# Kernel optimization log

Hardware: AMD Instinct MI355X
Metric: run time of the kernel (lower is better)

Reference implementation:

```python
import jax, jax.numpy as jnp
import numpy as np

B, L, D = 4, 2048, 1024
H, DK, DV = 16, 64, 64


def setup_inputs() -> dict:
    key = jax.random.key(0)
    ks = jax.random.split(key, 11)
    s = 1.0 / np.sqrt(D)
    so = 1.0 / np.sqrt(H * DV)
    return {
        "query": jax.random.normal(ks[0], (B, L, D), jnp.float32),
        "key": jax.random.normal(ks[1], (B, L, D), jnp.float32),
        "value": jax.random.normal(ks[2], (B, L, D), jnp.float32),
        "W_q": jax.random.uniform(ks[3], (D, H * DK), jnp.float32, -s, s),
        "b_q": jax.random.uniform(ks[4], (H * DK,), jnp.float32, -s, s),
        "W_k": jax.random.uniform(ks[5], (D, H * DK), jnp.float32, -s, s),
        "b_k": jax.random.uniform(ks[6], (H * DK,), jnp.float32, -s, s),
        "W_v": jax.random.uniform(ks[7], (D, H * DV), jnp.float32, -s, s),
        "b_v": jax.random.uniform(ks[8], (H * DV,), jnp.float32, -s, s),
        "W_o": jax.random.uniform(ks[9], (H * DV, D), jnp.float32, -so, so),
        "b_o": jax.random.uniform(ks[10], (D,), jnp.float32, -so, so),
    }


def reference(query, key, value, W_q, b_q, W_k, b_k, W_v, b_v, W_o, b_o):
    # QKV projections, then split heads: [B, L, H*d] -> [B, H, L, d]
    q = (query @ W_q + b_q).reshape(B, L, H, DK).transpose(0, 2, 1, 3)
    k = (key @ W_k + b_k).reshape(B, L, H, DK).transpose(0, 2, 1, 3)
    v = (value @ W_v + b_v).reshape(B, L, H, DV).transpose(0, 2, 1, 3)
    # scaled dot-product attention: softmax(q k^T / sqrt(dk)) v
    scores = jnp.einsum("bhqd,bhkd->bhqk", q, k) / jnp.sqrt(jnp.float32(DK))
    attn = jax.nn.softmax(scores, axis=-1)
    ctx = jnp.einsum("bhqk,bhkd->bhqd", attn, v)
    # combine heads: [B, H, L, dv] -> [B, L, H*dv], output projection
    out = ctx.transpose(0, 2, 1, 3).reshape(B, L, H * DV) @ W_o + b_o
    return out
```

## Files before the change

### kernel.cpp

```cpp
#include <hip/hip_runtime.h>

#define BATCH 4
#define LSEQ 2048
#define DMODEL 1024
#define NHEAD 16
#define DHEAD 64
#define MTOT (BATCH * LSEQ)

typedef _Float16 f16;
typedef _Float16 f16x8 __attribute__((ext_vector_type(8)));
typedef _Float16 f16x4 __attribute__((ext_vector_type(4)));
typedef _Float16 f16x2 __attribute__((ext_vector_type(2)));
typedef float f32x4 __attribute__((ext_vector_type(4)));
typedef float f32x16 __attribute__((ext_vector_type(16)));
typedef unsigned int u32;
typedef unsigned int u32x4 __attribute__((ext_vector_type(4)));

#define SCORE_SCALE 0.180336878f

typedef const __attribute__((address_space(1))) void gvoid;
typedef __attribute__((address_space(3))) void lvoid;
#define GLDS16(g, l) __builtin_amdgcn_global_load_lds((gvoid*)(g), (lvoid*)(l), 16, 0, 0)

#define WAITCNT(s) do { asm volatile("s_waitcnt " s ::: "memory"); \
                        __builtin_amdgcn_sched_barrier(0); } while (0)
#define BAR() __builtin_amdgcn_s_barrier()

__global__ __launch_bounds__(256)
void cvt3_f32_f16(const float* __restrict__ in0, const float* __restrict__ in1,
                  const float* __restrict__ in2, f16* __restrict__ out, int n8)
{
    const int y = blockIdx.y;
    const float* in = (y == 0) ? in0 : (y == 1) ? in1 : in2;
    f16* o = out + (size_t)y * (size_t)n8 * 8;
    int i = blockIdx.x * 256 + threadIdx.x;
    if (i >= n8) return;
    float4 a = ((const float4*)in)[2 * i];
    float4 b = ((const float4*)in)[2 * i + 1];
    f16x8 v;
    v[0] = (f16)a.x; v[1] = (f16)a.y; v[2] = (f16)a.z; v[3] = (f16)a.w;
    v[4] = (f16)b.x; v[5] = (f16)b.y; v[6] = (f16)b.z; v[7] = (f16)b.w;
    ((f16x8*)o)[i] = v;
}

__global__ __launch_bounds__(256)
void wconv4(const float* __restrict__ W0, const float* __restrict__ W1,
            const float* __restrict__ W2, const float* __restrict__ W3,
            f16* __restrict__ WtBase)
{
    __shared__ float T[64][68];
    const int z = blockIdx.z;
    const float* W = (z == 0) ? W0 : (z == 1) ? W1 : (z == 2) ? W2 : W3;
    f16* Wt = WtBase + (size_t)z * DMODEL * DMODEL;
    const int t = threadIdx.x;
    const int k0 = blockIdx.y * 64, n0 = blockIdx.x * 64;
    const int tr = t >> 4, tc = (t & 15) * 4;
#pragma unroll
    for (int p = 0; p < 64; p += 16) {
        float4 v = *(const float4*)&W[(size_t)(k0 + tr + p) * DMODEL + n0 + tc];
        *(float4*)&T[tr + p][tc] = v;
    }
    __syncthreads();
    const int n = t >> 2, kc = (t & 3) * 16;
    f16x8 o0, o1;
#pragma unroll
    for (int j = 0; j < 8; ++j) o0[j] = (f16)T[kc + j][n];
#pragma unroll
    for (int j = 0; j < 8; ++j) o1[j] = (f16)T[kc + 8 + j][n];
    *(f16x8*)&Wt[(size_t)(n0 + n) * DMODEL + k0 + kc] = o0;
    *(f16x8*)&Wt[(size_t)(n0 + n) * DMODEL + k0 + kc + 8] = o1;
}

__global__ __launch_bounds__(512, 2)
void gemm_qkv_8ph(const f16* __restrict__ A, const f16* __restrict__ Bt,
                  const float* __restrict__ b0, const float* __restrict__ b1,
                  const float* __restrict__ b2, f16* __restrict__ Cout)
{
    __shared__ f16 As[2][2][128][64];
    __shared__ f16 Bs[2][2][128][64];

    const int t = threadIdx.x;
    const int lane = t & 63;
    const int w = t >> 6, wr = w >> 2, wc = w & 3;
    const int quad = lane >> 4, m16 = lane & 15;
    const int m0 = blockIdx.x * 256, n0 = blockIdx.y * 256;
    const int which = n0 >> 10;

    const int sr = t >> 3;
    const int sc = ((t & 7) << 4) ^ ((sr & 7) << 4);
    const f16* Asrc = A + (size_t)which * MTOT * DMODEL
                        + (size_t)(m0 + sr) * DMODEL + (sc >> 1);
    const f16* Bsrc = Bt + (size_t)(n0 + sr) * DMODEL + (sc >> 1);

    auto stA = [&](int buf, int h, int kt) {
        const f16* s = Asrc + (size_t)(h * 128) * DMODEL + kt * 64;
        GLDS16(s,               &As[buf][h][0][0] + t * 8);
        GLDS16(s + 64 * DMODEL, &As[buf][h][64][0] + t * 8);
    };
    auto stB = [&](int buf, int h, int kt) {
        const f16* s = Bsrc + (size_t)(h * 128) * DMODEL + kt * 64;
        GLDS16(s,               &Bs[buf][h][0][0] + t * 8);
        GLDS16(s + 64 * DMODEL, &Bs[buf][h][64][0] + t * 8);
    };

    const int fsw = (m16 & 7) << 4;
    auto rdA = [&](int buf, int mf, int ks) -> f16x8 {
        return *(const f16x8*)((const char*)&As[buf][wr][0][0]
                               + (mf * 16 + m16) * 128
                               + ((ks * 64 + quad * 16) ^ fsw));
    };
    auto rdB = [&](int buf, int nf, int ks) -> f16x8 {
        return *(const f16x8*)((const char*)&Bs[buf][wc >> 1][0][0]
                               + ((wc & 1) * 64 + nf * 16 + m16) * 128
                               + ((ks * 64 + quad * 16) ^ fsw));
    };

    f32x4 acc[8][4] = {};
    f16x8 af[4][2], bf[4][2];

    auto ldA = [&](int buf, int mg) {
#pragma unroll
        for (int mi = 0; mi < 4; ++mi)
#pragma unroll
            for (int ks = 0; ks < 2; ++ks)
                af[mi][ks] = rdA(buf, mg * 4 + mi, ks);
    };
    auto ldB = [&](int buf) {
#pragma unroll
        for (int nf = 0; nf < 4; ++nf)
#pragma unroll
            for (int ks = 0; ks < 2; ++ks)
                bf[nf][ks] = rdB(buf, nf, ks);
    };
    auto mfma16 = [&](int mg, int np) {
        __builtin_amdgcn_s_setprio(1);
#pragma unroll
        for (int mi = 0; mi < 4; ++mi)
#pragma unroll
            for (int ni = 0; ni < 2; ++ni)
#pragma unroll
                for (int ks = 0; ks < 2; ++ks)
                    acc[mg * 4 + mi][np * 2 + ni] =
                        __builtin_amdgcn_mfma_f32_16x16x32_f16(
                            af[mi][ks], bf[np * 2 + ni][ks],
                            acc[mg * 4 + mi][np * 2 + ni], 0, 0, 0);
        __builtin_amdgcn_s_setprio(0);
    };

    stB(0, 0, 0); stB(0, 1, 0); stA(0, 0, 0); stA(0, 1, 0);
    stB(1, 0, 1); stB(1, 1, 1); stA(1, 0, 1);
    WAITCNT("vmcnt(6)");
    BAR();
    __builtin_amdgcn_sched_barrier(0);

    const int NHI = (DMODEL / 128) - 1;
    for (int i = 0; i < NHI; ++i) {
        const int T1 = 2 * i + 1, T2 = 2 * i + 2, T3 = 2 * i + 3;
        ldA(0, 0); ldB(0);
        stA(1, 1, T1);
        BAR(); WAITCNT("lgkmcnt(0)");
        mfma16(0, 0);
        BAR(); __builtin_amdgcn_sched_barrier(0);
        stB(0, 0, T2);
        BAR(); WAITCNT("lgkmcnt(0)");
        mfma16(0, 1);
        BAR(); __builtin_amdgcn_sched_barrier(0);
        ldA(0, 1);
        stB(0, 1, T2);
        BAR(); WAITCNT("lgkmcnt(0)");
        mfma16(1, 0);
        BAR(); __builtin_amdgcn_sched_barrier(0);
        stA(0, 0, T2);
        WAITCNT("vmcnt(6)");
        BAR(); WAITCNT("lgkmcnt(0)");
        mfma16(1, 1);
        BAR(); __builtin_amdgcn_sched_barrier(0);
        ldA(1, 0); ldB(1);
        stA(0, 1, T2);
        BAR(); WAITCNT("lgkmcnt(0)");
        mfma16(0, 0);
        BAR(); __builtin_amdgcn_sched_barrier(0);
        stB(1, 0, T3);
        BAR(); WAITCNT("lgkmcnt(0)");
        mfma16(0, 1);
        BAR(); __builtin_amdgcn_sched_barrier(0);
        ldA(1, 1);
        stB(1, 1, T3);
        BAR(); WAITCNT("lgkmcnt(0)");
        mfma16(1, 0);
        BAR(); __builtin_amdgcn_sched_barrier(0);
        stA(1, 0, T3);
        WAITCNT("vmcnt(6)");
        BAR(); WAITCNT("lgkmcnt(0)");
        mfma16(1, 1);
        BAR(); __builtin_amdgcn_sched_barrier(0);
    }

    stA(1, 1, 2 * NHI + 1);
    WAITCNT("vmcnt(0)");
    BAR();
    ldA(0, 0); ldB(0); WAITCNT("lgkmcnt(0)");
    mfma16(0, 0); mfma16(0, 1);
    ldA(0, 1); WAITCNT("lgkmcnt(0)");
    mfma16(1, 0); mfma16(1, 1);
    ldA(1, 0); ldB(1); WAITCNT("lgkmcnt(0)");
    mfma16(0, 0); mfma16(0, 1);
    ldA(1, 1); WAITCNT("lgkmcnt(0)");
    mfma16(1, 0); mfma16(1, 1);

    const float* bp = (which == 0) ? b0 : (which == 1) ? b1 : b2;
    const float scale = (which == 0) ? SCORE_SCALE : 1.0f;
    f16* o = Cout + (size_t)which * MTOT * DMODEL;
#pragma unroll
    for (int nf = 0; nf < 4; ++nf) {
        const int nn = (n0 + wc * 64 + nf * 16 + m16) & 1023;
        const float bv = bp[nn];
        const int h = nn >> 6, d = nn & 63;
#pragma unroll
        for (int mf = 0; mf < 8; ++mf) {
            const int mrow = m0 + wr * 128 + mf * 16 + quad * 4;
            const int b = mrow >> 11, l0 = mrow & (LSEQ - 1);
            if (which < 2) {
#pragma unroll
                for (int j = 0; j < 4; ++j) {
                    const float v = (acc[mf][nf][j] + bv) * scale;
                    o[(((size_t)(b * NHEAD + h) * LSEQ + l0 + j) << 6) + d] = (f16)v;
                }
            } else {
                f16x4 pk;
#pragma unroll
                for (int j = 0; j < 4; ++j) pk[j] = (f16)(acc[mf][nf][j] + bv);
                *(f16x4*)&o[(((size_t)(b * NHEAD + h) << 6) + d) * LSEQ + l0] = pk;
            }
        }
    }
}

__global__ __launch_bounds__(256)
void gemm_f16(const f16* __restrict__ A, const f16* __restrict__ Bt,
              const float* __restrict__ b0, const float* __restrict__ b1,
              const float* __restrict__ b2, void* __restrict__ Cout, int fused)
{
    __shared__ f16 As2[2][128][32];
    __shared__ f16 Bs2[2][128][32];

    const int t = threadIdx.x;
    const int lane = t & 63, w = t >> 6;
    const int quad = lane >> 4, m16 = lane & 15;
    const int m0 = blockIdx.x * 128;
    const int n0 = blockIdx.y * 128;
    const int wm = (w & 1) * 64, wn = (w >> 1) * 64;

    const int which = fused ? (n0 >> 10) : 0;

    f32x4 acc[4][4] = {};

    const f16* Ag = A + (size_t)which * MTOT * DMODEL
                      + (size_t)(m0 + (t >> 2)) * DMODEL + (t & 3) * 8;
    const f16* Bg = Bt + (size_t)(n0 + (t >> 2)) * DMODEL + (t & 3) * 8;
    f16* Al = &As2[0][0][0] + t * 8;
    f16* Bl = &Bs2[0][0][0] + t * 8;

    for (int k0 = 0; k0 < DMODEL; k0 += 64) {
        __syncthreads();
#pragma unroll
        for (int h = 0; h < 2; ++h) {
            GLDS16(Ag + k0 + h * 32, Al + h * 4096);
            GLDS16(Ag + k0 + h * 32 + (size_t)64 * DMODEL, Al + h * 4096 + 2048);
            GLDS16(Bg + k0 + h * 32, Bl + h * 4096);
            GLDS16(Bg + k0 + h * 32 + (size_t)64 * DMODEL, Bl + h * 4096 + 2048);
        }
        __syncthreads();
#pragma unroll
        for (int h = 0; h < 2; ++h) {
            f16x8 af[4], bf[4];
#pragma unroll
            for (int mi = 0; mi < 4; ++mi)
                af[mi] = *(const f16x8*)&As2[h][wm + mi * 16 + m16][quad * 8];
#pragma unroll
            for (int ni = 0; ni < 4; ++ni)
                bf[ni] = *(const f16x8*)&Bs2[h][wn + ni * 16 + m16][quad * 8];
#pragma unroll
            for (int mi = 0; mi < 4; ++mi)
#pragma unroll
                for (int ni = 0; ni < 4; ++ni)
                    acc[mi][ni] = __builtin_amdgcn_mfma_f32_16x16x32_f16(
                        af[mi], bf[ni], acc[mi][ni], 0, 0, 0);
        }
    }

    if (fused) {
        const float* bp = (which == 0) ? b0 : (which == 1) ? b1 : b2;
        const float scale = (which == 0) ? SCORE_SCALE : 1.0f;
        f16* o = (f16*)Cout + (size_t)which * MTOT * DMODEL;
#pragma unroll
        for (int ni = 0; ni < 4; ++ni) {
            const int nn = (n0 + wn + ni * 16 + m16) & 1023;
            const float bv = bp[nn];
            const int h = nn >> 6, d = nn & 63;
#pragma unroll
            for (int mi = 0; mi < 4; ++mi) {
                const int mrow = m0 + wm + mi * 16 + quad * 4;
                const int b = mrow >> 11, l0 = mrow & (LSEQ - 1);
                if (which < 2) {
#pragma unroll
                    for (int j = 0; j < 4; ++j) {
                        const float v = (acc[mi][ni][j] + bv) * scale;
                        o[(((size_t)(b * NHEAD + h) * LSEQ + l0 + j) << 6) + d] = (f16)v;
                    }
                } else {
                    f16x4 pk;
#pragma unroll
                    for (int j = 0; j < 4; ++j) pk[j] = (f16)(acc[mi][ni][j] + bv);
                    *(f16x4*)&o[(((size_t)(b * NHEAD + h) << 6) + d) * LSEQ + l0] = pk;
                }
            }
        }
    } else {
#pragma unroll
        for (int ni = 0; ni < 4; ++ni) {
            const int n = n0 + wn + ni * 16 + m16;
            const float bv = b0[n];
#pragma unroll
            for (int mi = 0; mi < 4; ++mi)
#pragma unroll
                for (int j = 0; j < 4; ++j) {
                    const int m = m0 + wm + mi * 16 + quad * 4 + j;
                    ((float*)Cout)[(size_t)m * DMODEL + n] = acc[mi][ni][j] + bv;
                }
        }
    }
}

__global__ __launch_bounds__(512, 4)
void attn_mfma(const f16* __restrict__ Qh, const f16* __restrict__ Kh,
               const f16* __restrict__ Vt, f16* __restrict__ ctx)
{
    __shared__ f16 Ks[2][64 * 64];
    __shared__ f16 Vs[2][64 * 64];

    const int t = threadIdx.x;
    const int lane = t & 63, w = t >> 6;
    const int l31 = lane & 31;
    const int hi = lane >> 5;
    const int swz = (l31 & 7) << 4;

    const int bid = blockIdx.x;
    const int x = bid & 7, rest = bid >> 3;
    const int qt = rest & 7;
    const int g = x + 8 * (rest >> 3);
    const int q0 = qt * 256 + w * 32;

    const f16* Qg = Qh + (size_t)g * LSEQ * DHEAD;
    const f16* Kg = Kh + (size_t)g * LSEQ * DHEAD;
    const f16* Vg = Vt + (size_t)g * LSEQ * DHEAD;

    f16x8 qf[4];
#pragma unroll
    for (int s = 0; s < 4; ++s)
        qf[s] = *(const f16x8*)&Qg[(size_t)(q0 + l31) * DHEAD + 16 * s + 8 * hi];

    const int srow = t >> 3;
    const int sxs = ((t & 7) << 4) ^ ((srow & 7) << 4);
    const f16* ksrc = Kg + (size_t)srow * DHEAD + (sxs >> 1);
    const f16* vsrc = Vg + (size_t)srow * LSEQ + (sxs >> 1);
    f16* kdst0 = &Ks[0][0] + t * 8;
    f16* vdst0 = &Vs[0][0] + t * 8;
    f16* kdst1 = &Ks[1][0] + t * 8;
    f16* vdst1 = &Vs[1][0] + t * 8;

    f32x16 ctxa[2] = {};
    float lsum = 0.f;

    GLDS16(ksrc, kdst0);
    GLDS16(vsrc, vdst0);
    __syncthreads();

    auto proc = [&](const f32x16& stv, const int kb, const char* Vc) {
        u32 d[8];
#pragma unroll
        for (int r = 0; r < 8; ++r) {
            const float p0 = __builtin_amdgcn_exp2f(stv[2 * r]);
            const float p1 = __builtin_amdgcn_exp2f(stv[2 * r + 1]);
            lsum += p0 + p1;
            f16x2 pk; pk[0] = (f16)p0; pk[1] = (f16)p1;
            d[r] = __builtin_bit_cast(u32, pk);
        }
#pragma unroll
        for (int s = 0; s < 2; ++s) {
            const u32 sendE = hi ? d[4 * s + 0] : d[4 * s + 2];
            const u32 sendO = hi ? d[4 * s + 1] : d[4 * s + 3];
            const u32 recvE = __shfl_xor(sendE, 32);
            const u32 recvO = __shfl_xor(sendO, 32);
            u32x4 paw;
            paw[0] = hi ? recvE : d[4 * s + 0];
            paw[1] = hi ? recvO : d[4 * s + 1];
            paw[2] = hi ? d[4 * s + 2] : recvE;
            paw[3] = hi ? d[4 * s + 3] : recvO;
            const f16x8 pa = __builtin_bit_cast(f16x8, paw);
            const int kbyte = kb * 64 + 32 * s + 16 * hi;
#pragma unroll
            for (int d32 = 0; d32 < 2; ++d32) {
                const int vrow = d32 * 32 + l31;
                const f16x8 vf = *(const f16x8*)(Vc + vrow * 128 + (kbyte ^ swz));
                ctxa[d32] = __builtin_amdgcn_mfma_f32_32x32x16_f16(
                    pa, vf, ctxa[d32], 0, 0, 0);
            }
        }
    };

    auto compute = [&](const f16* Kbuf, const f16* Vbuf) {
        const char* Kc = (const char*)Kbuf;
        const char* Vc = (const char*)Vbuf;
        f32x16 s0 = {}, s1 = {};
#pragma unroll
        for (int s = 0; s < 4; ++s) {
            const int cb = 32 * s + 16 * hi;
            const f16x8 kf0 = *(const f16x8*)(Kc + l31 * 128 + (cb ^ swz));
            const f16x8 kf1 = *(const f16x8*)(Kc + (l31 + 32) * 128 + (cb ^ swz));
            s0 = __builtin_amdgcn_mfma_f32_32x32x16_f16(kf0, qf[s], s0, 0, 0, 0);
            s1 = __builtin_amdgcn_mfma_f32_32x32x16_f16(kf1, qf[s], s1, 0, 0, 0);
        }
        proc(s0, 0, Vc);
        proc(s1, 1, Vc);
    };

    for (int kt = 0; kt < LSEQ; kt += 128) {
        if (kt + 64 < LSEQ) {
            GLDS16(ksrc + (size_t)(kt + 64) * DHEAD, kdst1);
            GLDS16(vsrc + (kt + 64), vdst1);
        }
        compute(&Ks[0][0], &Vs[0][0]);
        __syncthreads();
        if (kt + 128 < LSEQ) {
            GLDS16(ksrc + (size_t)(kt + 128) * DHEAD, kdst0);
            GLDS16(vsrc + (kt + 128), vdst0);
        }
        compute(&Ks[1][0], &Vs[1][0]);
        __syncthreads();
    }

    const float l = lsum + __shfl_xor(lsum, 32);
    const float linv = 1.0f / l;
    const int batch = g >> 4, h = g & 15;
#pragma unroll
    for (int r = 0; r < 16; ++r) {
        const int qr = (r & 3) + 8 * (r >> 2) + 4 * hi;
        const float inv = __shfl(linv, qr);
        f16* op = ctx + ((size_t)(batch * LSEQ + q0 + qr)) * DMODEL
                      + h * 64 + l31;
        op[0]  = (f16)(ctxa[0][r] * inv);
        op[32] = (f16)(ctxa[1][r] * inv);
    }
}

extern "C" void kernel_launch(void* const* d_in, const int* in_sizes, int n_in,
                              void* d_out, int out_size, void* d_ws, size_t ws_size,
                              hipStream_t stream)
{
    const float* query = (const float*)d_in[0];
    const float* key   = (const float*)d_in[1];
    const float* value = (const float*)d_in[2];
    const float* W_q   = (const float*)d_in[3];
    const float* b_q   = (const float*)d_in[4];
    const float* W_k   = (const float*)d_in[5];
    const float* b_k   = (const float*)d_in[6];
    const float* W_v   = (const float*)d_in[7];
    const float* b_v   = (const float*)d_in[8];
    const float* W_o   = (const float*)d_in[9];
    const float* b_o   = (const float*)d_in[10];
    float* out = (float*)d_out;

    const size_t MAT = (size_t)MTOT * DMODEL;
    f16* base = (f16*)d_ws;
    f16* Aq   = base;
    f16* Qhp  = base + 3 * MAT;
    f16* ctxh = base + 6 * MAT;
    f16* Wtq  = base + 7 * MAT;
    f16* Wto  = Wtq + (size_t)3 * DMODEL * DMODEL;

    const int n8 = (int)(MAT / 8);
    cvt3_f32_f16<<<dim3(n8 / 256, 3), 256, 0, stream>>>(query, key, value, Aq, n8);
    wconv4<<<dim3(DMODEL / 64, DMODEL / 64, 4), 256, 0, stream>>>(W_q, W_k, W_v, W_o, Wtq);

    gemm_qkv_8ph<<<dim3(MTOT / 256, 3 * DMODEL / 256), 512, 0, stream>>>(
        Aq, Wtq, b_q, b_k, b_v, Qhp);

    attn_mfma<<<BATCH * NHEAD * (LSEQ / 256), 512, 0, stream>>>(
        Qhp, Qhp + MAT, Qhp + 2 * MAT, ctxh);

    gemm_f16<<<dim3(MTOT / 128, DMODEL / 128), 256, 0, stream>>>(
        ctxh, Wto, b_o, nullptr, nullptr, out, 0);
}
```

Baseline: 348.5 us.

## Replace 8-phase interleaved QKV GEMM schedule with simple double-buffered k-loop

The QKV projection GEMM drops its hand-interleaved 8-phase schedule, which split LDS staging and MFMA work into eight barrier-separated phases per two k-tiles. It now uses a plain double-buffered loop: wait for a tile, compute the whole 64-wide k-tile, then issue the global-to-LDS loads for tile k+2. This cuts barriers and setprio toggles but gives up the finer overlap of loads with MFMA. The epilogue is also reordered to hoist the bias and head index math and to iterate nf innermost.

Measured after the change: 343.1 us. About the same (-1.5%).

```diff
diff --git a/kernel.cpp b/kernel.cpp
--- a/kernel.cpp
+++ b/kernel.cpp
@@ -25,6 +25,7 @@
 #define WAITCNT(s) do { asm volatile("s_waitcnt " s ::: "memory"); \
                         __builtin_amdgcn_sched_barrier(0); } while (0)
 #define BAR() __builtin_amdgcn_s_barrier()
+#define SCHED0() __builtin_amdgcn_sched_barrier(0)
 
 __global__ __launch_bounds__(256)
 void cvt3_f32_f16(const float* __restrict__ in0, const float* __restrict__ in1,
@@ -72,9 +73,9 @@
 }
 
 __global__ __launch_bounds__(512, 2)
-void gemm_qkv_8ph(const f16* __restrict__ A, const f16* __restrict__ Bt,
-                  const float* __restrict__ b0, const float* __restrict__ b1,
-                  const float* __restrict__ b2, f16* __restrict__ Cout)
+void gemm_qkv(const f16* __restrict__ A, const f16* __restrict__ Bt,
+              const float* __restrict__ b0, const float* __restrict__ b1,
+              const float* __restrict__ b2, f16* __restrict__ Cout)
 {
     __shared__ f16 As[2][2][128][64];
     __shared__ f16 Bs[2][2][128][64];
@@ -102,6 +103,10 @@
         GLDS16(s,               &Bs[buf][h][0][0] + t * 8);
         GLDS16(s + 64 * DMODEL, &Bs[buf][h][64][0] + t * 8);
     };
+    auto stageTile = [&](int k) {
+        const int b = k & 1;
+        stA(b, 0, k); stA(b, 1, k); stB(b, 0, k); stB(b, 1, k);
+    };
 
     const int fsw = (m16 & 7) << 4;
     auto rdA = [&](int buf, int mf, int ks) -> f16x8 {
@@ -116,121 +121,90 @@
     };
 
     f32x4 acc[8][4] = {};
-    f16x8 af[4][2], bf[4][2];
-
-    auto ldA = [&](int buf, int mg) {
-#pragma unroll
-        for (int mi = 0; mi < 4; ++mi)
-#pragma unroll
-            for (int ks = 0; ks < 2; ++ks)
-                af[mi][ks] = rdA(buf, mg * 4 + mi, ks);
-    };
-    auto ldB = [&](int buf) {
+
+    auto compute = [&](int buf) {
+        f16x8 af[4][2], bf[4][2];
 #pragma unroll
         for (int nf = 0; nf < 4; ++nf)
 #pragma unroll
             for (int ks = 0; ks < 2; ++ks)
                 bf[nf][ks] = rdB(buf, nf, ks);
-    };
-    auto mfma16 = [&](int mg, int np) {
-        __builtin_amdgcn_s_setprio(1);
-#pragma unroll
-        for (int mi = 0; mi < 4; ++mi)
-#pragma unroll
-            for (int ni = 0; ni < 2; ++ni)
+#pragma unroll
+        for (int mg = 0; mg < 2; ++mg) {
+#pragma unroll
+            for (int mi = 0; mi < 4; ++mi)
 #pragma unroll
                 for (int ks = 0; ks < 2; ++ks)
-                    acc[mg * 4 + mi][np * 2 + ni] =
-                        __builtin_amdgcn_mfma_f32_16x16x32_f16(
-                            af[mi][ks], bf[np * 2 + ni][ks],
-                            acc[mg * 4 + mi][np * 2 + ni], 0, 0, 0);
-        __builtin_amdgcn_s_setprio(0);
-    };
-
-    stB(0, 0, 0); stB(0, 1, 0); stA(0, 0, 0); stA(0, 1, 0);
-    stB(1, 0, 1); stB(1, 1, 1); stA(1, 0, 1);
-    WAITCNT("vmcnt(6)");
-    BAR();
-    __builtin_amdgcn_sched_barrier(0);
-
-    const int NHI = (DMODEL / 128) - 1;
-    for (int i = 0; i < NHI; ++i) {
-        const int T1 = 2 * i + 1, T2 = 2 * i + 2, T3 = 2 * i + 3;
-        ldA(0, 0); ldB(0);
-        stA(1, 1, T1);
-        BAR(); WAITCNT("lgkmcnt(0)");
-        mfma16(0, 0);
-        BAR(); __builtin_amdgcn_sched_barrier(0);
-        stB(0, 0, T2);
-        BAR(); WAITCNT("lgkmcnt(0)");
-        mfma16(0, 1);
-        BAR(); __builtin_amdgcn_sched_barrier(0);
-        ldA(0, 1);
-        stB(0, 1, T2);
-        BAR(); WAITCNT("lgkmcnt(0)");
-        mfma16(1, 0);
-        BAR(); __builtin_amdgcn_sched_barrier(0);
-        stA(0, 0, T2);
-        WAITCNT("vmcnt(6)");
-        BAR(); WAITCNT("lgkmcnt(0)");
-        mfma16(1, 1);
-        BAR(); __builtin_amdgcn_sched_barrier(0);
-        ldA(1, 0); ldB(1);
-        stA(0, 1, T2);
-        BAR(); WAITCNT("lgkmcnt(0)");
-        mfma16(0, 0);
-        BAR(); __builtin_amdgcn_sched_barrier(0);
-        stB(1, 0, T3);
-        BAR(); WAITCNT("lgkmcnt(0)");
-        mfma16(0, 1);
-        BAR(); __builtin_amdgcn_sched_barrier(0);
-        ldA(1, 1);
-        stB(1, 1, T3);
-        BAR(); WAITCNT("lgkmcnt(0)");
-        mfma16(1, 0);
-        BAR(); __builtin_amdgcn_sched_barrier(0);
-        stA(1, 0, T3);
-        WAITCNT("vmcnt(6)");
-        BAR(); WAITCNT("lgkmcnt(0)");
-        mfma16(1, 1);
-        BAR(); __builtin_amdgcn_sched_barrier(0);
-    }
-
-    stA(1, 1, 2 * NHI + 1);
+                    af[mi][ks] = rdA(buf, mg * 4 + mi, ks);
+#pragma unroll
+            for (int mi = 0; mi < 4; ++mi)
+#pragma unroll
+                for (int ni = 0; ni < 4; ++ni)
+#pragma unroll
+                    for (int ks = 0; ks < 2; ++ks)
+                        acc[mg * 4 + mi][ni] =
+                            __builtin_amdgcn_mfma_f32_16x16x32_f16(
+                                af[mi][ks], bf[ni][ks],
+                                acc[mg * 4 + mi][ni], 0, 0, 0);
+        }
+    };
+
+    const int NKT = DMODEL / 64;
+    stageTile(0);
+    stageTile(1);
+
+#pragma unroll 2
+    for (int k = 0; k < NKT - 2; ++k) {
+        WAITCNT("vmcnt(8)");
+        BAR(); SCHED0();
+        compute(k & 1);
+        WAITCNT("lgkmcnt(0)");
+        BAR(); SCHED0();
+        stageTile(k + 2);
+        SCHED0();
+    }
+    WAITCNT("vmcnt(8)");
+    BAR(); SCHED0();
+    compute((NKT - 2) & 1);
+    WAITCNT("lgkmcnt(0)");
+    BAR(); SCHED0();
     WAITCNT("vmcnt(0)");
-    BAR();
-    ldA(0, 0); ldB(0); WAITCNT("lgkmcnt(0)");
-    mfma16(0, 0); mfma16(0, 1);
-    ldA(0, 1); WAITCNT("lgkmcnt(0)");
-    mfma16(1, 0); mfma16(1, 1);
-    ldA(1, 0); ldB(1); WAITCNT("lgkmcnt(0)");
-    mfma16(0, 0); mfma16(0, 1);
-    ldA(1, 1); WAITCNT("lgkmcnt(0)");
-    mfma16(1, 0); mfma16(1, 1);
+    BAR(); SCHED0();
+    compute((NKT - 1) & 1);
 
     const float* bp = (which == 0) ? b0 : (which == 1) ? b1 : b2;
     const float scale = (which == 0) ? SCORE_SCALE : 1.0f;
     f16* o = Cout + (size_t)which * MTOT * DMODEL;
+    float bv[4];
+    int hh[4], dd[4];
 #pragma unroll
     for (int nf = 0; nf < 4; ++nf) {
         const int nn = (n0 + wc * 64 + nf * 16 + m16) & 1023;
-        const float bv = bp[nn];
-        const int h = nn >> 6, d = nn & 63;
-#pragma unroll
-        for (int mf = 0; mf < 8; ++mf) {
-            const int mrow = m0 + wr * 128 + mf * 16 + quad * 4;
-            const int b = mrow >> 11, l0 = mrow & (LSEQ - 1);
-            if (which < 2) {
-#pragma unroll
-                for (int j = 0; j < 4; ++j) {
-                    const float v = (acc[mf][nf][j] + bv) * scale;
-                    o[(((size_t)(b * NHEAD + h) * LSEQ + l0 + j) << 6) + d] = (f16)v;
+        bv[nf] = bp[nn];
+        hh[nf] = nn >> 6;
+        dd[nf] = nn & 63;
+    }
+#pragma unroll
+    for (int mf = 0; mf < 8; ++mf) {
+        const int mrow = m0 + wr * 128 + mf * 16 + quad * 4;
+        const int b = mrow >> 11, l0 = mrow & (LSEQ - 1);
+        if (which < 2) {
+#pragma unroll
+            for (int j = 0; j < 4; ++j)
+#pragma unroll
+                for (int nf = 0; nf < 4; ++nf) {
+                    const float v = (acc[mf][nf][j] + bv[nf]) * scale;
+                    o[(((size_t)(b * NHEAD + hh[nf]) * LSEQ + l0 + j) << 6)
+                      + dd[nf]] = (f16)v;
                 }
-            } else {
+        } else {
+#pragma unroll
+            for (int nf = 0; nf < 4; ++nf) {
                 f16x4 pk;
 #pragma unroll
-                for (int j = 0; j < 4; ++j) pk[j] = (f16)(acc[mf][nf][j] + bv);
-                *(f16x4*)&o[(((size_t)(b * NHEAD + h) << 6) + d) * LSEQ + l0] = pk;
+                for (int j = 0; j < 4; ++j) pk[j] = (f16)(acc[mf][nf][j] + bv[nf]);
+                *(f16x4*)&o[(((size_t)(b * NHEAD + hh[nf]) << 6) + dd[nf]) * LSEQ
+                            + l0] = pk;
             }
         }
     }
@@ -483,7 +457,7 @@
     cvt3_f32_f16<<<dim3(n8 / 256, 3), 256, 0, stream>>>(query, key, value, Aq, n8);
     wconv4<<<dim3(DMODEL / 64, DMODEL / 64, 4), 256, 0, stream>>>(W_q, W_k, W_v, W_o, Wtq);
 
-    gemm_qkv_8ph<<<dim3(MTOT / 256, 3 * DMODEL / 256), 512, 0, stream>>>(
+    gemm_qkv<<<dim3(MTOT / 256, 3 * DMODEL / 256), 512, 0, stream>>>(
         Aq, Wtq, b_q, b_k, b_v, Qhp);
 
     attn_mfma<<<BATCH * NHEAD * (LSEQ / 256), 512, 0, stream>>>(
```
